# Kernel optimization log

Measured on AMD Instinct MI355X. Metric: run time of the kernel, lower is better.

The kernel has to match this reference:

```python
import jax, jax.numpy as jnp
import numpy as np

N_NODES = 100000
N_EDGES = 6400000
TOKEN_DIM = 16


def setup_inputs() -> dict:
    key = jax.random.key(0)
    k1, k2, k3, k4, k5 = jax.random.split(key, 5)
    x = jax.random.normal(k1, (N_NODES, 1), dtype=jnp.float32)
    edge_index = jax.random.randint(k2, (2, N_EDGES), 0, N_NODES, dtype=jnp.int64)
    # PyTorch nn.Linear init: U(-1/sqrt(fan_in), 1/sqrt(fan_in)); plain normals are fine for a correctness baseline
    w1 = jax.random.normal(k3, (TOKEN_DIM, 2), dtype=jnp.float32) * (1.0 / np.sqrt(2.0))
    b1 = jnp.zeros((TOKEN_DIM,), dtype=jnp.float32)
    w2 = jax.random.normal(k4, (TOKEN_DIM, TOKEN_DIM), dtype=jnp.float32) * (1.0 / np.sqrt(TOKEN_DIM))
    b2 = jnp.zeros((TOKEN_DIM,), dtype=jnp.float32)
    return {"x": x, "edge_index": edge_index, "w1": w1, "b1": b1, "w2": w2, "b2": b2}


def reference(x, edge_index, w1, b1, w2, b2):
    row, col = edge_index[0], edge_index[1]
    # gather-multiply: bond_e = s_row * s_col, shape [E, 1]
    bond = x[row] * x[col]
    # scatter-add into local_field, shape [N, 1]
    local_field = jax.ops.segment_sum(bond, row, num_segments=x.shape[0])
    feats = jnp.concatenate([x, local_field], axis=1)  # [N, 2]
    h = jax.nn.relu(feats @ w1.T + b1)                  # [N, token_dim]
    tokens = jax.nn.relu(h @ w2.T + b2)                 # [N, token_dim]
    return tokens
```

## Files before the change

kernel.cpp:

```cpp
#include <hip/hip_runtime.h>

#define TOKEN_DIM 16
#define RANGES 5
#define MAX_RS 20000
#define MAX_C  102

__global__ __launch_bounds__(1024, 8)
void nit_phase1(const int* __restrict__ row, const int* __restrict__ col,
                const float* __restrict__ x,
                float* __restrict__ partial,
                int N, long long E, int chunkE, int RS) {
    __shared__ float acc[MAX_RS];
    const int c = blockIdx.x / RANGES;
    const int r = blockIdx.x % RANGES;
    const int base = r * RS;
    int cnt = N - base; if (cnt > RS) cnt = RS; if (cnt < 0) cnt = 0;
    const int t = threadIdx.x, nt = blockDim.x;

    for (int j = t; j < cnt; j += nt) acc[j] = 0.0f;
    __syncthreads();

    long long i0 = (long long)c * chunkE;
    long long i1 = i0 + chunkE; if (i1 > E) i1 = E;
    if (i0 < i1) {
        long long len = i1 - i0;
        long long ngrp = len >> 3;
        for (long long g = t; g < ngrp; g += nt) {
            long long idx = i0 + (g << 3);
            int4 r0 = *reinterpret_cast<const int4*>(row + idx);
            int4 r1 = *reinterpret_cast<const int4*>(row + idx + 4);
            int4 c0 = *reinterpret_cast<const int4*>(col + idx);
            int4 c1 = *reinterpret_cast<const int4*>(col + idx + 4);
            unsigned d;
            d = (unsigned)(r0.x - base); if (d < (unsigned)cnt) atomicAdd(&acc[d], x[c0.x]);
            d = (unsigned)(r0.y - base); if (d < (unsigned)cnt) atomicAdd(&acc[d], x[c0.y]);
            d = (unsigned)(r0.z - base); if (d < (unsigned)cnt) atomicAdd(&acc[d], x[c0.z]);
            d = (unsigned)(r0.w - base); if (d < (unsigned)cnt) atomicAdd(&acc[d], x[c0.w]);
            d = (unsigned)(r1.x - base); if (d < (unsigned)cnt) atomicAdd(&acc[d], x[c1.x]);
            d = (unsigned)(r1.y - base); if (d < (unsigned)cnt) atomicAdd(&acc[d], x[c1.y]);
            d = (unsigned)(r1.z - base); if (d < (unsigned)cnt) atomicAdd(&acc[d], x[c1.z]);
            d = (unsigned)(r1.w - base); if (d < (unsigned)cnt) atomicAdd(&acc[d], x[c1.w]);
        }
        for (long long idx = i0 + (ngrp << 3) + t; idx < i1; idx += nt) {
            unsigned d = (unsigned)(row[idx] - base);
            if (d < (unsigned)cnt) atomicAdd(&acc[d], x[col[idx]]);
        }
    }
    __syncthreads();

    float* dst = partial + (size_t)c * N + base;
    for (int j = t; j < cnt; j += nt) dst[j] = acc[j];
}

__global__ __launch_bounds__(256, 8)
void nit_phase2(const float* __restrict__ x,
                const float* __restrict__ partial,
                const float* __restrict__ w1, const float* __restrict__ b1,
                const float* __restrict__ w2, const float* __restrict__ b2,
                float* __restrict__ out, int N, int C) {
    __shared__ float sw1[TOKEN_DIM * 2];
    __shared__ float sb1[TOKEN_DIM];
    __shared__ float sw2[TOKEN_DIM * TOKEN_DIM];
    __shared__ float sb2[TOKEN_DIM];
    __shared__ float red[256];

    const int t = threadIdx.x;
    if (t < TOKEN_DIM * TOKEN_DIM) sw2[t] = w2[t];
    if (t < TOKEN_DIM * 2) sw1[t] = w1[t];
    if (t < TOKEN_DIM) { sb1[t] = b1[t]; sb2[t] = b2[t]; }

    const int n = t & 63;
    const int g = t >> 6;
    const int node0 = blockIdx.x * 64;
    const int node = node0 + n;

    float s = 0.0f;
    if (node < N) {
        for (int c = g; c < C; c += 4) s += partial[(size_t)c * N + node];
    }
    red[t] = s;
    __syncthreads();

    if (t < 64) {
        const int nn = node0 + t;
        if (nn < N) {
            const float ssum = red[t] + red[64 + t] + red[128 + t] + red[192 + t];
            const float xv = x[nn];
            const float lv = xv * ssum;

            float h[TOKEN_DIM];
#pragma unroll
            for (int j = 0; j < TOKEN_DIM; ++j) {
                float v = fmaf(xv, sw1[2 * j], fmaf(lv, sw1[2 * j + 1], sb1[j]));
                h[j] = v > 0.0f ? v : 0.0f;
            }

            float o[TOKEN_DIM];
#pragma unroll
            for (int j = 0; j < TOKEN_DIM; ++j) {
                float v = sb2[j];
#pragma unroll
                for (int k = 0; k < TOKEN_DIM; ++k)
                    v = fmaf(h[k], sw2[j * TOKEN_DIM + k], v);
                o[j] = v > 0.0f ? v : 0.0f;
            }

            float4* op = reinterpret_cast<float4*>(out + (size_t)nn * TOKEN_DIM);
#pragma unroll
            for (int j = 0; j < 4; ++j)
                op[j] = make_float4(o[4 * j], o[4 * j + 1], o[4 * j + 2], o[4 * j + 3]);
        }
    }
}

extern "C" void kernel_launch(void* const* d_in, const int* in_sizes, int n_in,
                              void* d_out, int out_size, void* d_ws, size_t ws_size,
                              hipStream_t stream) {
    const float* x  = (const float*)d_in[0];
    const int*   ei = (const int*)d_in[1];
    const float* w1 = (const float*)d_in[2];
    const float* b1 = (const float*)d_in[3];
    const float* w2 = (const float*)d_in[4];
    const float* b2 = (const float*)d_in[5];
    float* out = (float*)d_out;

    const int N = in_sizes[0];
    const long long E = in_sizes[1] / 2;
    const int* row = ei;
    const int* col = ei + E;

    int maxC = (int)(ws_size / ((size_t)N * sizeof(float)));
    int C = maxC < 1 ? 1 : (maxC > MAX_C ? MAX_C : maxC);
    const int RS = (N + RANGES - 1) / RANGES;
    long long ce = (E + C - 1) / C;
    int chunkE = (int)((ce + 7LL) & ~7LL);

    float* partial = (float*)d_ws;

    nit_phase1<<<C * RANGES, 1024, 0, stream>>>(row, col, x, partial,
                                                N, E, chunkE, RS);

    int grid2 = (N + 63) / 64;
    nit_phase2<<<grid2, 256, 0, stream>>>(x, partial, w1, b1, w2, b2,
                                          out, N, C);
}
```

Measured before the change: 166.3 us.

## Store per-chunk partial sums as bf16 and unroll edge loads to 16

Phase 1 now writes its per-chunk partial node sums as bf16 with nontemporal stores, and phase 2 reads them back as bf16, widening them to float before reducing. This halves the workspace traffic between the two kernels. The edge loop now loads 16 row/col indices per thread per iteration instead of 8, and the chunk size is aligned to 16. The bf16 partials cut precision in the local field sum, which may push results past the correctness tolerance.

After: 163.5 us. Within noise of the previous version (-1.7%).

```diff
diff --git a/kernel.cpp b/kernel.cpp
--- a/kernel.cpp
+++ b/kernel.cpp
@@ -1,4 +1,5 @@
 #include <hip/hip_runtime.h>
+#include <hip/hip_bf16.h>
 
 #define TOKEN_DIM 16
 #define RANGES 5
@@ -8,7 +9,7 @@
 __global__ __launch_bounds__(1024, 8)
 void nit_phase1(const int* __restrict__ row, const int* __restrict__ col,
                 const float* __restrict__ x,
-                float* __restrict__ partial,
+                unsigned short* __restrict__ partial,
                 int N, long long E, int chunkE, int RS) {
     __shared__ float acc[MAX_RS];
     const int c = blockIdx.x / RANGES;
@@ -22,39 +23,54 @@
 
     long long i0 = (long long)c * chunkE;
     long long i1 = i0 + chunkE; if (i1 > E) i1 = E;
-    if (i0 < i1) {
-        long long len = i1 - i0;
-        long long ngrp = len >> 3;
-        for (long long g = t; g < ngrp; g += nt) {
-            long long idx = i0 + (g << 3);
-            int4 r0 = *reinterpret_cast<const int4*>(row + idx);
-            int4 r1 = *reinterpret_cast<const int4*>(row + idx + 4);
-            int4 c0 = *reinterpret_cast<const int4*>(col + idx);
-            int4 c1 = *reinterpret_cast<const int4*>(col + idx + 4);
-            unsigned d;
-            d = (unsigned)(r0.x - base); if (d < (unsigned)cnt) atomicAdd(&acc[d], x[c0.x]);
-            d = (unsigned)(r0.y - base); if (d < (unsigned)cnt) atomicAdd(&acc[d], x[c0.y]);
-            d = (unsigned)(r0.z - base); if (d < (unsigned)cnt) atomicAdd(&acc[d], x[c0.z]);
-            d = (unsigned)(r0.w - base); if (d < (unsigned)cnt) atomicAdd(&acc[d], x[c0.w]);
-            d = (unsigned)(r1.x - base); if (d < (unsigned)cnt) atomicAdd(&acc[d], x[c1.x]);
-            d = (unsigned)(r1.y - base); if (d < (unsigned)cnt) atomicAdd(&acc[d], x[c1.y]);
-            d = (unsigned)(r1.z - base); if (d < (unsigned)cnt) atomicAdd(&acc[d], x[c1.z]);
-            d = (unsigned)(r1.w - base); if (d < (unsigned)cnt) atomicAdd(&acc[d], x[c1.w]);
-        }
-        for (long long idx = i0 + (ngrp << 3) + t; idx < i1; idx += nt) {
-            unsigned d = (unsigned)(row[idx] - base);
-            if (d < (unsigned)cnt) atomicAdd(&acc[d], x[col[idx]]);
-        }
+    long long len = (i1 > i0) ? (i1 - i0) : 0;
+    long long ngrp = len >> 4;
+
+    for (long long g = t; g < ngrp; g += nt) {
+        const int* rp = row + i0 + (g << 4);
+        const int* cp = col + i0 + (g << 4);
+        int4 r0 = *reinterpret_cast<const int4*>(rp);
+        int4 r1 = *reinterpret_cast<const int4*>(rp + 4);
+        int4 r2 = *reinterpret_cast<const int4*>(rp + 8);
+        int4 r3 = *reinterpret_cast<const int4*>(rp + 12);
+        int4 c0 = *reinterpret_cast<const int4*>(cp);
+        int4 c1 = *reinterpret_cast<const int4*>(cp + 4);
+        int4 c2 = *reinterpret_cast<const int4*>(cp + 8);
+        int4 c3 = *reinterpret_cast<const int4*>(cp + 12);
+        unsigned d;
+        d = (unsigned)(r0.x - base); if (d < (unsigned)cnt) atomicAdd(&acc[d], x[c0.x]);
+        d = (unsigned)(r0.y - base); if (d < (unsigned)cnt) atomicAdd(&acc[d], x[c0.y]);
+        d = (unsigned)(r0.z - base); if (d < (unsigned)cnt) atomicAdd(&acc[d], x[c0.z]);
+        d = (unsigned)(r0.w - base); if (d < (unsigned)cnt) atomicAdd(&acc[d], x[c0.w]);
+        d = (unsigned)(r1.x - base); if (d < (unsigned)cnt) atomicAdd(&acc[d], x[c1.x]);
+        d = (unsigned)(r1.y - base); if (d < (unsigned)cnt) atomicAdd(&acc[d], x[c1.y]);
+        d = (unsigned)(r1.z - base); if (d < (unsigned)cnt) atomicAdd(&acc[d], x[c1.z]);
+        d = (unsigned)(r1.w - base); if (d < (unsigned)cnt) atomicAdd(&acc[d], x[c1.w]);
+        d = (unsigned)(r2.x - base); if (d < (unsigned)cnt) atomicAdd(&acc[d], x[c2.x]);
+        d = (unsigned)(r2.y - base); if (d < (unsigned)cnt) atomicAdd(&acc[d], x[c2.y]);
+        d = (unsigned)(r2.z - base); if (d < (unsigned)cnt) atomicAdd(&acc[d], x[c2.z]);
+        d = (unsigned)(r2.w - base); if (d < (unsigned)cnt) atomicAdd(&acc[d], x[c2.w]);
+        d = (unsigned)(r3.x - base); if (d < (unsigned)cnt) atomicAdd(&acc[d], x[c3.x]);
+        d = (unsigned)(r3.y - base); if (d < (unsigned)cnt) atomicAdd(&acc[d], x[c3.y]);
+        d = (unsigned)(r3.z - base); if (d < (unsigned)cnt) atomicAdd(&acc[d], x[c3.z]);
+        d = (unsigned)(r3.w - base); if (d < (unsigned)cnt) atomicAdd(&acc[d], x[c3.w]);
+    }
+    for (long long idx = i0 + (ngrp << 4) + t; idx < i1; idx += nt) {
+        unsigned d = (unsigned)(row[idx] - base);
+        if (d < (unsigned)cnt) atomicAdd(&acc[d], x[col[idx]]);
     }
     __syncthreads();
 
-    float* dst = partial + (size_t)c * N + base;
-    for (int j = t; j < cnt; j += nt) dst[j] = acc[j];
+    unsigned short* dst = partial + (size_t)c * N + base;
+    for (int j = t; j < cnt; j += nt) {
+        __hip_bfloat16 h = __float2bfloat16(acc[j]);
+        __builtin_nontemporal_store(*reinterpret_cast<unsigned short*>(&h), dst + j);
+    }
 }
 
 __global__ __launch_bounds__(256, 8)
 void nit_phase2(const float* __restrict__ x,
-                const float* __restrict__ partial,
+                const unsigned short* __restrict__ partial,
                 const float* __restrict__ w1, const float* __restrict__ b1,
                 const float* __restrict__ w2, const float* __restrict__ b2,
                 float* __restrict__ out, int N, int C) {
@@ -76,7 +92,11 @@
 
     float s = 0.0f;
     if (node < N) {
-        for (int c = g; c < C; c += 4) s += partial[(size_t)c * N + node];
+#pragma unroll 4
+        for (int c = g; c < C; c += 4) {
+            unsigned short u = __builtin_nontemporal_load(partial + (size_t)c * N + node);
+            s += __uint_as_float(((unsigned)u) << 16);
+        }
     }
     red[t] = s;
     __syncthreads();
@@ -129,13 +149,13 @@
     const int* row = ei;
     const int* col = ei + E;
 
-    int maxC = (int)(ws_size / ((size_t)N * sizeof(float)));
-    int C = maxC < 1 ? 1 : (maxC > MAX_C ? MAX_C : maxC);
+    long long maxC = (long long)(ws_size / ((size_t)N * sizeof(unsigned short)));
+    int C = maxC < 1 ? 1 : (maxC > MAX_C ? MAX_C : (int)maxC);
     const int RS = (N + RANGES - 1) / RANGES;
     long long ce = (E + C - 1) / C;
-    int chunkE = (int)((ce + 7LL) & ~7LL);
+    int chunkE = (int)((ce + 15LL) & ~15LL);
 
-    float* partial = (float*)d_ws;
+    unsigned short* partial = (unsigned short*)d_ws;
 
     nit_phase1<<<C * RANGES, 1024, 0, stream>>>(row, col, x, partial,
                                                 N, E, chunkE, RS);
```

## Partition edges into per-range fp16-packed buckets before shared-memory accumulation

Applied to the files above, without the earlier changes.

Replaces the single scatter pass, where every block streamed its whole edge chunk and discarded the edges outside its node range (about 5x redundant reads), with a partition kernel. That kernel reads the edges once, gathers x[col], and writes packed (local row, fp16 value) words into per-range buckets using wave ballots and a shared cursor. A second kernel accumulates the buckets into shared memory and writes fp16 partial sums, and the MLP kernel reads fewer partials plus an overflow array. This cuts global traffic but adds a kernel launch and a memset, and the fp16 packing of x and of the partials loses precision.

After: 213.5 us. 1.28x slower.

```diff
diff --git a/kernel.cpp b/kernel.cpp
--- a/kernel.cpp
+++ b/kernel.cpp
@@ -1,17 +1,95 @@
 #include <hip/hip_runtime.h>
+#include <hip/hip_fp16.h>
 
 #define TOKEN_DIM 16
 #define RANGES 5
 #define MAX_RS 20000
-#define MAX_C  102
+#define P_BLOCKS 512
+#define SEGS_PER_GROUP 16
+#define CAP_DEFAULT 3000
+
+typedef int v4i __attribute__((ext_vector_type(4)));
 
 __global__ __launch_bounds__(1024, 8)
-void nit_phase1(const int* __restrict__ row, const int* __restrict__ col,
-                const float* __restrict__ x,
-                float* __restrict__ partial,
-                int N, long long E, int chunkE, int RS) {
+void nit_partition(const int* __restrict__ row, const int* __restrict__ col,
+                   const float* __restrict__ x,
+                   unsigned* __restrict__ buckets,
+                   int* __restrict__ counts,
+                   float* __restrict__ overflow,
+                   long long E, int segE, int cap, int RS) {
+    __shared__ int cursor[RANGES];
+    const int p = blockIdx.x;
+    const int t = threadIdx.x;
+    const int lane = t & 63;
+    if (t < RANGES) cursor[t] = 0;
+    __syncthreads();
+
+    long long s0 = (long long)p * segE;
+    long long s1 = s0 + segE; if (s1 > E) s1 = E;
+
+    for (long long ib = s0; ib < s1; ib += (long long)blockDim.x * 4) {
+        long long i = ib + (long long)t * 4;
+        long long rem = s1 - i;
+        int nval = rem >= 4 ? 4 : (rem > 0 ? (int)rem : 0);
+
+        int rw[4] = {0, 0, 0, 0};
+        int cw[4] = {0, 0, 0, 0};
+        if (nval == 4) {
+            v4i rv = __builtin_nontemporal_load(reinterpret_cast<const v4i*>(row + i));
+            v4i cv = __builtin_nontemporal_load(reinterpret_cast<const v4i*>(col + i));
+            rw[0] = rv.x; rw[1] = rv.y; rw[2] = rv.z; rw[3] = rv.w;
+            cw[0] = cv.x; cw[1] = cv.y; cw[2] = cv.z; cw[3] = cv.w;
+        } else {
+            for (int q = 0; q < nval; ++q) { rw[q] = row[i + q]; cw[q] = col[i + q]; }
+        }
+
+        float xs[4];
+        xs[0] = x[cw[0]]; xs[1] = x[cw[1]]; xs[2] = x[cw[2]]; xs[3] = x[cw[3]];
+
+#pragma unroll
+        for (int q = 0; q < 4; ++q) {
+            int rr = -1, lrow = 0;
+            if (q < nval) {
+                rr = rw[q] / RS; if (rr > RANGES - 1) rr = RANGES - 1;
+                lrow = rw[q] - rr * RS;
+            }
+            int before = 0, mycnt = 0;
+#pragma unroll
+            for (int k = 0; k < RANGES; ++k) {
+                unsigned long long m = __ballot(rr == k);
+                if (rr == k)
+                    before = __builtin_amdgcn_mbcnt_hi((unsigned)(m >> 32),
+                              __builtin_amdgcn_mbcnt_lo((unsigned)m, 0));
+                if (lane == k) mycnt = (int)__popcll(m);
+            }
+            int mybase = 0;
+            if (lane < RANGES && mycnt > 0) mybase = atomicAdd(&cursor[lane], mycnt);
+            int base = __shfl(mybase, rr < 0 ? 0 : rr);
+            if (q < nval) {
+                int slot = base + before;
+                unsigned short hb = __half_as_ushort(__float2half_rn(xs[q]));
+                unsigned packed = ((unsigned)lrow << 16) | (unsigned)hb;
+                if (slot < cap)
+                    buckets[((size_t)p * RANGES + rr) * cap + slot] = packed;
+                else
+                    atomicAdd(&overflow[rw[q]], xs[q]);
+            }
+        }
+    }
+    __syncthreads();
+    if (t < RANGES) {
+        int cval = cursor[t]; if (cval > cap) cval = cap;
+        counts[p * RANGES + t] = cval;
+    }
+}
+
+__global__ __launch_bounds__(1024, 8)
+void nit_accum(const unsigned* __restrict__ buckets,
+               const int* __restrict__ counts,
+               unsigned short* __restrict__ partial,
+               int N, int cap, int RS) {
     __shared__ float acc[MAX_RS];
-    const int c = blockIdx.x / RANGES;
+    const int g = blockIdx.x / RANGES;
     const int r = blockIdx.x % RANGES;
     const int base = r * RS;
     int cnt = N - base; if (cnt > RS) cnt = RS; if (cnt < 0) cnt = 0;
@@ -20,44 +98,30 @@
     for (int j = t; j < cnt; j += nt) acc[j] = 0.0f;
     __syncthreads();
 
-    long long i0 = (long long)c * chunkE;
-    long long i1 = i0 + chunkE; if (i1 > E) i1 = E;
-    if (i0 < i1) {
-        long long len = i1 - i0;
-        long long ngrp = len >> 3;
-        for (long long g = t; g < ngrp; g += nt) {
-            long long idx = i0 + (g << 3);
-            int4 r0 = *reinterpret_cast<const int4*>(row + idx);
-            int4 r1 = *reinterpret_cast<const int4*>(row + idx + 4);
-            int4 c0 = *reinterpret_cast<const int4*>(col + idx);
-            int4 c1 = *reinterpret_cast<const int4*>(col + idx + 4);
-            unsigned d;
-            d = (unsigned)(r0.x - base); if (d < (unsigned)cnt) atomicAdd(&acc[d], x[c0.x]);
-            d = (unsigned)(r0.y - base); if (d < (unsigned)cnt) atomicAdd(&acc[d], x[c0.y]);
-            d = (unsigned)(r0.z - base); if (d < (unsigned)cnt) atomicAdd(&acc[d], x[c0.z]);
-            d = (unsigned)(r0.w - base); if (d < (unsigned)cnt) atomicAdd(&acc[d], x[c0.w]);
-            d = (unsigned)(r1.x - base); if (d < (unsigned)cnt) atomicAdd(&acc[d], x[c1.x]);
-            d = (unsigned)(r1.y - base); if (d < (unsigned)cnt) atomicAdd(&acc[d], x[c1.y]);
-            d = (unsigned)(r1.z - base); if (d < (unsigned)cnt) atomicAdd(&acc[d], x[c1.z]);
-            d = (unsigned)(r1.w - base); if (d < (unsigned)cnt) atomicAdd(&acc[d], x[c1.w]);
-        }
-        for (long long idx = i0 + (ngrp << 3) + t; idx < i1; idx += nt) {
-            unsigned d = (unsigned)(row[idx] - base);
-            if (d < (unsigned)cnt) atomicAdd(&acc[d], x[col[idx]]);
-        }
-    }
-    __syncthreads();
-
-    float* dst = partial + (size_t)c * N + base;
-    for (int j = t; j < cnt; j += nt) dst[j] = acc[j];
+    for (int s = 0; s < SEGS_PER_GROUP; ++s) {
+        const int p = g * SEGS_PER_GROUP + s;
+        const int m = counts[p * RANGES + r];
+        const unsigned* bp = buckets + ((size_t)p * RANGES + r) * cap;
+        for (int j = t; j < m; j += nt) {
+            unsigned e = bp[j];
+            float v = __half2float(__ushort_as_half((unsigned short)(e & 0xffffu)));
+            atomicAdd(&acc[e >> 16], v);
+        }
+    }
+    __syncthreads();
+
+    unsigned short* dst = partial + (size_t)g * N + base;
+    for (int j = t; j < cnt; j += nt)
+        dst[j] = __half_as_ushort(__float2half_rn(acc[j]));
 }
 
 __global__ __launch_bounds__(256, 8)
-void nit_phase2(const float* __restrict__ x,
-                const float* __restrict__ partial,
-                const float* __restrict__ w1, const float* __restrict__ b1,
-                const float* __restrict__ w2, const float* __restrict__ b2,
-                float* __restrict__ out, int N, int C) {
+void nit_mlp(const float* __restrict__ x,
+             const unsigned short* __restrict__ partial,
+             const float* __restrict__ overflow,
+             const float* __restrict__ w1, const float* __restrict__ b1,
+             const float* __restrict__ w2, const float* __restrict__ b2,
+             float* __restrict__ out, int N, int G) {
     __shared__ float sw1[TOKEN_DIM * 2];
     __shared__ float sb1[TOKEN_DIM];
     __shared__ float sw2[TOKEN_DIM * TOKEN_DIM];
@@ -70,13 +134,14 @@
     if (t < TOKEN_DIM) { sb1[t] = b1[t]; sb2[t] = b2[t]; }
 
     const int n = t & 63;
-    const int g = t >> 6;
+    const int gq = t >> 6;
     const int node0 = blockIdx.x * 64;
     const int node = node0 + n;
 
     float s = 0.0f;
     if (node < N) {
-        for (int c = g; c < C; c += 4) s += partial[(size_t)c * N + node];
+        for (int c = gq; c < G; c += 4)
+            s += __half2float(__ushort_as_half(partial[(size_t)c * N + node]));
     }
     red[t] = s;
     __syncthreads();
@@ -84,7 +149,8 @@
     if (t < 64) {
         const int nn = node0 + t;
         if (nn < N) {
-            const float ssum = red[t] + red[64 + t] + red[128 + t] + red[192 + t];
+            const float ssum = red[t] + red[64 + t] + red[128 + t] + red[192 + t]
+                             + overflow[nn];
             const float xv = x[nn];
             const float lv = xv * ssum;
 
@@ -94,7 +160,6 @@
                 float v = fmaf(xv, sw1[2 * j], fmaf(lv, sw1[2 * j + 1], sb1[j]));
                 h[j] = v > 0.0f ? v : 0.0f;
             }
-
             float o[TOKEN_DIM];
 #pragma unroll
             for (int j = 0; j < TOKEN_DIM; ++j) {
@@ -104,7 +169,6 @@
                     v = fmaf(h[k], sw2[j * TOKEN_DIM + k], v);
                 o[j] = v > 0.0f ? v : 0.0f;
             }
-
             float4* op = reinterpret_cast<float4*>(out + (size_t)nn * TOKEN_DIM);
 #pragma unroll
             for (int j = 0; j < 4; ++j)
@@ -129,18 +193,34 @@
     const int* row = ei;
     const int* col = ei + E;
 
-    int maxC = (int)(ws_size / ((size_t)N * sizeof(float)));
-    int C = maxC < 1 ? 1 : (maxC > MAX_C ? MAX_C : maxC);
     const int RS = (N + RANGES - 1) / RANGES;
-    long long ce = (E + C - 1) / C;
-    int chunkE = (int)((ce + 7LL) & ~7LL);
-
-    float* partial = (float*)d_ws;
-
-    nit_phase1<<<C * RANGES, 1024, 0, stream>>>(row, col, x, partial,
-                                                N, E, chunkE, RS);
-
-    int grid2 = (N + 63) / 64;
-    nit_phase2<<<grid2, 256, 0, stream>>>(x, partial, w1, b1, w2, b2,
-                                          out, N, C);
-}
+    const int P  = P_BLOCKS;
+    const int G  = P / SEGS_PER_GROUP;
+    int segE = (int)(((E + P - 1) / P + 3) & ~3LL);
+
+    size_t countsB  = (size_t)P * RANGES * sizeof(int);
+    size_t overB    = (size_t)N * sizeof(float);
+    size_t partB    = (size_t)G * N * sizeof(unsigned short);
+    size_t fixedB   = ((countsB + 15) & ~15ULL) + ((overB + 15) & ~15ULL)
+                    + ((partB + 15) & ~15ULL) + 64;
+    long long capLL = (long long)((ws_size > fixedB ? ws_size - fixedB : 0)
+                                  / ((size_t)P * RANGES * sizeof(unsigned)));
+    int cap = capLL > CAP_DEFAULT ? CAP_DEFAULT : (capLL < 64 ? 64 : (int)capLL);
+
+    unsigned* buckets = (unsigned*)d_ws;
+    size_t off = ((size_t)P * RANGES * cap * sizeof(unsigned) + 15) & ~15ULL;
+    int* counts = (int*)((char*)d_ws + off);
+    off += (countsB + 15) & ~15ULL;
+    float* overflow = (float*)((char*)d_ws + off);
+    off += (overB + 15) & ~15ULL;
+    unsigned short* partial = (unsigned short*)((char*)d_ws + off);
+
+    hipMemsetAsync(overflow, 0, overB, stream);
+
+    nit_partition<<<P, 1024, 0, stream>>>(row, col, x, buckets, counts,
+                                          overflow, E, segE, cap, RS);
+    nit_accum<<<G * RANGES, 1024, 0, stream>>>(buckets, counts, partial,
+                                               N, cap, RS);
+    nit_mlp<<<(N + 63) / 64, 256, 0, stream>>>(x, partial, overflow,
+                                               w1, b1, w2, b2, out, N, G);
+}
```

## Store per-chunk partial sums in fp16 and make LDS atomics branch-free

Applied to the files above, without the earlier changes.

Phase-one partial sums are written as fp16 rather than fp32, halving the workspace traffic in both the write and the phase-two reduction, and the workspace can now hold more chunks. Out-of-range edges are redirected to a dummy LDS slot so every atomic executes unconditionally, and all eight x gathers are hoisted ahead of the atomics to overlap their loads. The fp16 rounding of partial sums adds accuracy loss and a risk of overflow, while the dummy slot turns every out-of-range edge into a heavily contended atomic on one address.

New measurement: 308.3 us. 1.85x slower.

```diff
diff --git a/kernel.cpp b/kernel.cpp
--- a/kernel.cpp
+++ b/kernel.cpp
@@ -1,4 +1,5 @@
 #include <hip/hip_runtime.h>
+#include <hip/hip_fp16.h>
 
 #define TOKEN_DIM 16
 #define RANGES 5
@@ -8,53 +9,57 @@
 __global__ __launch_bounds__(1024, 8)
 void nit_phase1(const int* __restrict__ row, const int* __restrict__ col,
                 const float* __restrict__ x,
-                float* __restrict__ partial,
+                unsigned short* __restrict__ partial,
                 int N, long long E, int chunkE, int RS) {
-    __shared__ float acc[MAX_RS];
+    __shared__ float acc[MAX_RS + 1];
     const int c = blockIdx.x / RANGES;
     const int r = blockIdx.x % RANGES;
     const int base = r * RS;
     int cnt = N - base; if (cnt > RS) cnt = RS; if (cnt < 0) cnt = 0;
     const int t = threadIdx.x, nt = blockDim.x;
 
-    for (int j = t; j < cnt; j += nt) acc[j] = 0.0f;
+    for (int j = t; j <= MAX_RS; j += nt) acc[j] = 0.0f;
     __syncthreads();
 
     long long i0 = (long long)c * chunkE;
     long long i1 = i0 + chunkE; if (i1 > E) i1 = E;
-    if (i0 < i1) {
-        long long len = i1 - i0;
-        long long ngrp = len >> 3;
-        for (long long g = t; g < ngrp; g += nt) {
-            long long idx = i0 + (g << 3);
-            int4 r0 = *reinterpret_cast<const int4*>(row + idx);
-            int4 r1 = *reinterpret_cast<const int4*>(row + idx + 4);
-            int4 c0 = *reinterpret_cast<const int4*>(col + idx);
-            int4 c1 = *reinterpret_cast<const int4*>(col + idx + 4);
-            unsigned d;
-            d = (unsigned)(r0.x - base); if (d < (unsigned)cnt) atomicAdd(&acc[d], x[c0.x]);
-            d = (unsigned)(r0.y - base); if (d < (unsigned)cnt) atomicAdd(&acc[d], x[c0.y]);
-            d = (unsigned)(r0.z - base); if (d < (unsigned)cnt) atomicAdd(&acc[d], x[c0.z]);
-            d = (unsigned)(r0.w - base); if (d < (unsigned)cnt) atomicAdd(&acc[d], x[c0.w]);
-            d = (unsigned)(r1.x - base); if (d < (unsigned)cnt) atomicAdd(&acc[d], x[c1.x]);
-            d = (unsigned)(r1.y - base); if (d < (unsigned)cnt) atomicAdd(&acc[d], x[c1.y]);
-            d = (unsigned)(r1.z - base); if (d < (unsigned)cnt) atomicAdd(&acc[d], x[c1.z]);
-            d = (unsigned)(r1.w - base); if (d < (unsigned)cnt) atomicAdd(&acc[d], x[c1.w]);
-        }
-        for (long long idx = i0 + (ngrp << 3) + t; idx < i1; idx += nt) {
-            unsigned d = (unsigned)(row[idx] - base);
-            if (d < (unsigned)cnt) atomicAdd(&acc[d], x[col[idx]]);
-        }
+    long long len = (i1 > i0) ? (i1 - i0) : 0;
+    long long ngrp = len >> 3;
+
+    for (long long g = t; g < ngrp; g += nt) {
+        const int* rp = row + i0 + (g << 3);
+        const int* cp = col + i0 + (g << 3);
+        int4 r0 = *reinterpret_cast<const int4*>(rp);
+        int4 r1 = *reinterpret_cast<const int4*>(rp + 4);
+        int4 c0 = *reinterpret_cast<const int4*>(cp);
+        int4 c1 = *reinterpret_cast<const int4*>(cp + 4);
+        float x0 = x[c0.x], x1 = x[c0.y], x2 = x[c0.z], x3 = x[c0.w];
+        float x4 = x[c1.x], x5 = x[c1.y], x6 = x[c1.z], x7 = x[c1.w];
+        unsigned d; int a;
+        d = (unsigned)(r0.x - base); a = d < (unsigned)cnt ? (int)d : MAX_RS; atomicAdd(&acc[a], x0);
+        d = (unsigned)(r0.y - base); a = d < (unsigned)cnt ? (int)d : MAX_RS; atomicAdd(&acc[a], x1);
+        d = (unsigned)(r0.z - base); a = d < (unsigned)cnt ? (int)d : MAX_RS; atomicAdd(&acc[a], x2);
+        d = (unsigned)(r0.w - base); a = d < (unsigned)cnt ? (int)d : MAX_RS; atomicAdd(&acc[a], x3);
+        d = (unsigned)(r1.x - base); a = d < (unsigned)cnt ? (int)d : MAX_RS; atomicAdd(&acc[a], x4);
+        d = (unsigned)(r1.y - base); a = d < (unsigned)cnt ? (int)d : MAX_RS; atomicAdd(&acc[a], x5);
+        d = (unsigned)(r1.z - base); a = d < (unsigned)cnt ? (int)d : MAX_RS; atomicAdd(&acc[a], x6);
+        d = (unsigned)(r1.w - base); a = d < (unsigned)cnt ? (int)d : MAX_RS; atomicAdd(&acc[a], x7);
+    }
+    for (long long idx = i0 + (ngrp << 3) + t; idx < i1; idx += nt) {
+        unsigned d = (unsigned)(row[idx] - base);
+        int a = d < (unsigned)cnt ? (int)d : MAX_RS;
+        atomicAdd(&acc[a], x[col[idx]]);
     }
     __syncthreads();
 
-    float* dst = partial + (size_t)c * N + base;
-    for (int j = t; j < cnt; j += nt) dst[j] = acc[j];
+    unsigned short* dst = partial + (size_t)c * N + base;
+    for (int j = t; j < cnt; j += nt)
+        dst[j] = __half_as_ushort(__float2half_rn(acc[j]));
 }
 
 __global__ __launch_bounds__(256, 8)
 void nit_phase2(const float* __restrict__ x,
-                const float* __restrict__ partial,
+                const unsigned short* __restrict__ partial,
                 const float* __restrict__ w1, const float* __restrict__ b1,
                 const float* __restrict__ w2, const float* __restrict__ b2,
                 float* __restrict__ out, int N, int C) {
@@ -76,7 +81,9 @@
 
     float s = 0.0f;
     if (node < N) {
-        for (int c = g; c < C; c += 4) s += partial[(size_t)c * N + node];
+#pragma unroll 4
+        for (int c = g; c < C; c += 4)
+            s += __half2float(__ushort_as_half(partial[(size_t)c * N + node]));
     }
     red[t] = s;
     __syncthreads();
@@ -129,13 +136,13 @@
     const int* row = ei;
     const int* col = ei + E;
 
-    int maxC = (int)(ws_size / ((size_t)N * sizeof(float)));
-    int C = maxC < 1 ? 1 : (maxC > MAX_C ? MAX_C : maxC);
+    long long maxC = (long long)(ws_size / ((size_t)N * sizeof(unsigned short)));
+    int C = maxC < 1 ? 1 : (maxC > MAX_C ? MAX_C : (int)maxC);
     const int RS = (N + RANGES - 1) / RANGES;
     long long ce = (E + C - 1) / C;
     int chunkE = (int)((ce + 7LL) & ~7LL);
 
-    float* partial = (float*)d_ws;
+    unsigned short* partial = (unsigned short*)d_ws;
 
     nit_phase1<<<C * RANGES, 1024, 0, stream>>>(row, col, x, partial,
                                                 N, E, chunkE, RS);
```
